# Kernel optimization log

Hardware: AMD Instinct MI355X
Metric: run time of the kernel (lower is better)

## Reference

```python
import jax, jax.numpy as jnp
import numpy as np

WIN = 256  # window_size from init_kwargs


def _stream_attn(q, k, v, win, hollow):
    """Banded sliding-window attention.

    hollow=False (s-stream): key j attended iff 0 <= i - j < win (last `win` tokens incl. self).
    hollow=True  (c-stream): key j attended iff win <= i - j < 2*win (tokens [i-2W+1, i-W]).
    Returns (out [B,S,H,D], lse [B,H,S]) with lse = -inf for fully-masked rows.
    """
    B, S, H, D = q.shape
    nb = S // win
    scale = D ** -0.5
    qb = q.reshape(B, nb, win, H, D)
    kb = k.reshape(B, nb, win, H, D)
    vb = v.reshape(B, nb, win, H, D)
    pad = ((0, 0), (2, 0), (0, 0), (0, 0), (0, 0))
    kp = jnp.pad(kb, pad)
    vp = jnp.pad(vb, pad)
    k_ctx = jnp.concatenate([kp[:, t:t + nb] for t in range(3)], axis=2)  # [B,nb,3W,H,D]
    v_ctx = jnp.concatenate([vp[:, t:t + nb] for t in range(3)], axis=2)
    lq = jnp.arange(win)[:, None]
    kk = jnp.arange(3 * win)[None, :]
    t_blk = kk // win
    lk = kk % win
    rel = (2 - t_blk) * win + lq - lk  # i - j, shape [W, 3W]
    if hollow:
        wmask = (rel >= win) & (rel < 2 * win)
    else:
        wmask = (rel >= 0) & (rel < win)
    blk_ok = (jnp.arange(nb)[:, None] - 2 + (jnp.arange(3 * win) // win)[None, :]) >= 0  # [nb,3W]
    mask = wmask[None] & blk_ok[:, None, :]  # [nb, W, 3W]
    logits = jnp.einsum('bnqhd,bnkhd->bnhqk', qb, k_ctx) * scale  # [B,nb,H,W,3W]
    logits = jnp.where(mask[None, :, None], logits, -jnp.inf)
    m = jnp.max(logits, axis=-1)  # [B,nb,H,W]
    ms = jnp.where(jnp.isneginf(m), 0.0, m)
    p = jnp.exp(logits - ms[..., None])
    denom = jnp.sum(p, axis=-1)  # [B,nb,H,W]
    out = jnp.einsum('bnhqk,bnkhd->bnqhd', p, v_ctx)  # [B,nb,W,H,D]
    safe = jnp.where(denom > 0, denom, 1.0)
    out = out / jnp.moveaxis(safe, 2, 3)[..., None]
    lse = jnp.where(denom > 0, jnp.log(safe) + m, -jnp.inf)  # [B,nb,H,W]
    out = out.reshape(B, S, H, D)
    lse = jnp.moveaxis(lse, 1, 2).reshape(B, H, S)
    return out, lse


def _merge(out_c, lse_c, out_s, lse_s):
    # faithful jax version of merge_attn_states_torch (LSE online-softmax merge)
    m = jnp.maximum(lse_c, lse_s)
    ms = jnp.where(jnp.isneginf(m), 0.0, m)
    ec = jnp.exp(lse_c - ms)
    es = jnp.exp(lse_s - ms)
    se = ec + es  # s-stream always has >=1 key (self), so se > 0
    c_scale = jnp.moveaxis(ec / se, 1, 2)[..., None]  # [B,S,H,1]
    s_scale = jnp.moveaxis(es / se, 1, 2)[..., None]
    return out_c * c_scale + out_s * s_scale


def setup_inputs() -> dict:
    key = jax.random.key(0)
    k1, k2, k3 = jax.random.split(key, 3)
    B, S, H, D = 2, 2048, 16, 128
    return {
        'query': jax.random.normal(k1, (B, S, H, D), dtype=jnp.float32),
        'key': jax.random.normal(k2, (B, S, H, D), dtype=jnp.float32),
        'value': jax.random.normal(k3, (B, S, H, D), dtype=jnp.float32),
    }


def reference(query, key, value):
    out_c, lse_c = _stream_attn(query, key, value, WIN, hollow=True)   # c-stream: [i-2W, i-W]
    out_s, lse_s = _stream_attn(query, key, value, WIN, hollow=False)  # s-stream: last W tokens
    return _merge(out_c, lse_c, out_s, lse_s)
```

## Files before the change

### kernel.cpp

```cpp
#include <hip/hip_runtime.h>
#include <math.h>

#define S_LEN 2048
#define NH    16
#define DD    128
#define SROW  (NH*DD)
#define WIN2  512
#define BQ    128
#define BK    64
#define RSQ   136
#define RS    72

typedef __bf16 bf16x8 __attribute__((ext_vector_type(8)));
typedef __bf16 bf16x4 __attribute__((ext_vector_type(4)));
typedef float  f32x4  __attribute__((ext_vector_type(4)));

__device__ __forceinline__ f32x4 mfma16(bf16x8 a, bf16x8 b, f32x4 c) {
    return __builtin_amdgcn_mfma_f32_16x16x32_bf16(a, b, c, 0, 0, 0);
}

__device__ __forceinline__ unsigned int pack_bf16(float lo, float hi) {
    return (unsigned int)__builtin_bit_cast(unsigned short, (__bf16)lo)
         | ((unsigned int)__builtin_bit_cast(unsigned short, (__bf16)hi) << 16);
}

#define OFF_VT 8704
#define OFF_P  17920
#define SMEM_ELEMS 27136

__global__ __launch_bounds__(256, 2)
void swattn_kernel(const float* __restrict__ Qg, const float* __restrict__ Kg,
                   const float* __restrict__ Vg, float* __restrict__ Og) {
    __shared__ __align__(16) __bf16 smem[SMEM_ELEMS];

    const int t   = threadIdx.x;
    const int w   = t >> 6;
    const int l   = t & 63;
    const int r16 = l & 15;
    const int g4  = l >> 4;
    const int qt  = blockIdx.x;
    const int h   = blockIdx.y;
    const int b   = blockIdx.z;
    const int Qlo = qt * BQ;

    const size_t bh = ((size_t)b * S_LEN) * SROW + (size_t)h * DD;

    for (int it = 0; it < 16; ++it) {
        int f   = it * 256 + t;
        int q_l = f >> 5;
        int dq  = (f & 31) * 4;
        const float4 v = *(const float4*)&Qg[bh + (size_t)(Qlo + q_l) * SROW + dq];
        bf16x4 o4 = { (__bf16)v.x, (__bf16)v.y, (__bf16)v.z, (__bf16)v.w };
        *(bf16x4*)&smem[q_l * RSQ + dq] = o4;
    }
    __syncthreads();

    bf16x8 qf[2][4];
#pragma unroll
    for (int qg = 0; qg < 2; ++qg)
#pragma unroll
        for (int sl = 0; sl < 4; ++sl)
            qf[qg][sl] = *(const bf16x8*)&smem[(w*32 + qg*16 + r16) * RSQ + sl*32 + g4*8];
    __syncthreads();

    const f32x4 zero4 = {0.f, 0.f, 0.f, 0.f};
    f32x4 oacc[8][2];
#pragma unroll
    for (int dg = 0; dg < 8; ++dg) { oacc[dg][0] = zero4; oacc[dg][1] = zero4; }
    float m_run[2] = { -1e30f, -1e30f };
    float l_run[2] = { 0.f, 0.f };

    const int q_lo_w = Qlo + w * 32;
    const int q_hi_w = q_lo_w + 31;
    const float C1 = 0.08838834764831845f * 1.44269504088896340f;

    int cb = Qlo - (WIN2 - 1);
    if (cb < 0) cb = 0;
    cb &= ~(BK - 1);
    const int Qhi = Qlo + BQ - 1;

    for (int c0 = cb; c0 <= Qhi; c0 += BK) {
        for (int it = 0; it < 8; ++it) {
            int f   = it * 256 + t;
            int k_l = f >> 5;
            int dq  = (f & 31) * 4;
            const float4 v = *(const float4*)&Kg[bh + (size_t)(c0 + k_l) * SROW + dq];
            bf16x4 o4 = { (__bf16)v.x, (__bf16)v.y, (__bf16)v.z, (__bf16)v.w };
            *(bf16x4*)&smem[k_l * RSQ + dq] = o4;
        }
        {
            const int gv = l >> 5;
            const int rv = l & 31;
            for (int it = 0; it < 8; ++it) {
                int k0l = w * 16 + it * 2;
                const float4 v4 = *(const float4*)&Vg[bh + (size_t)(c0 + k0l + gv) * SROW + 4*rv];
                float ox = __shfl_xor(v4.x, 32);
                float oy = __shfl_xor(v4.y, 32);
                float oz = __shfl_xor(v4.z, 32);
                float ow = __shfl_xor(v4.w, 32);
                float lo0, hi0, lo1, hi1; int d0;
                if (gv == 0) { lo0 = v4.x; hi0 = ox;   lo1 = v4.y; hi1 = oy;   d0 = 4*rv; }
                else         { lo0 = oz;   hi0 = v4.z; lo1 = ow;   hi1 = v4.w; d0 = 4*rv + 2; }
                *(unsigned int*)&smem[OFF_VT + (d0    ) * RS + k0l] = pack_bf16(lo0, hi0);
                *(unsigned int*)&smem[OFF_VT + (d0 + 1) * RS + k0l] = pack_bf16(lo1, hi1);
            }
        }
        __syncthreads();

        const bool act = (q_hi_w >= c0) && (q_lo_w <= c0 + (BK - 1) + (WIN2 - 1));
        if (act) {
            f32x4 st[4][2];
#pragma unroll
            for (int kg = 0; kg < 4; ++kg) { st[kg][0] = zero4; st[kg][1] = zero4; }
#pragma unroll
            for (int sl = 0; sl < 4; ++sl)
#pragma unroll
                for (int kg = 0; kg < 4; ++kg) {
                    bf16x8 kf = *(const bf16x8*)&smem[(kg*16 + r16) * RSQ + sl*32 + g4*8];
                    st[kg][0] = mfma16(kf, qf[0][sl], st[kg][0]);
                    st[kg][1] = mfma16(kf, qf[1][sl], st[kg][1]);
                }

            const bool fv = (q_lo_w >= c0 + (BK - 1)) && (q_hi_w <= c0 + (WIN2 - 1));
            if (fv) {
#pragma unroll
                for (int kg = 0; kg < 4; ++kg)
#pragma unroll
                    for (int qg = 0; qg < 2; ++qg)
#pragma unroll
                        for (int rg = 0; rg < 4; ++rg) st[kg][qg][rg] *= C1;
            } else {
#pragma unroll
                for (int qg = 0; qg < 2; ++qg) {
                    int iq = q_lo_w + qg*16 + r16;
#pragma unroll
                    for (int kg = 0; kg < 4; ++kg) {
                        int relb = iq - (c0 + kg*16 + 4*g4);
#pragma unroll
                        for (int rg = 0; rg < 4; ++rg) {
                            bool ok = ((unsigned)(relb - rg)) < (unsigned)WIN2;
                            st[kg][qg][rg] = ok ? st[kg][qg][rg] * C1 : -1e30f;
                        }
                    }
                }
            }

            float alpha[2];
#pragma unroll
            for (int qg = 0; qg < 2; ++qg) {
                float mc = -1e30f;
#pragma unroll
                for (int kg = 0; kg < 4; ++kg)
#pragma unroll
                    for (int rg = 0; rg < 4; ++rg) mc = fmaxf(mc, st[kg][qg][rg]);
                mc = fmaxf(mc, __shfl_xor(mc, 16));
                mc = fmaxf(mc, __shfl_xor(mc, 32));
                float mn = fmaxf(m_run[qg], mc);
                alpha[qg] = exp2f(m_run[qg] - mn);
                m_run[qg] = mn;
                float sum = 0.f;
#pragma unroll
                for (int kg = 0; kg < 4; ++kg)
#pragma unroll
                    for (int rg = 0; rg < 4; ++rg) {
                        float tv = st[kg][qg][rg];
                        float p  = exp2f(tv - mn);
                        if (!fv) p = (tv > -1e29f) ? p : 0.f;
                        st[kg][qg][rg] = p;
                        sum += p;
                    }
                sum += __shfl_xor(sum, 16);
                sum += __shfl_xor(sum, 32);
                l_run[qg] = l_run[qg] * alpha[qg] + sum;
            }

#pragma unroll
            for (int qg = 0; qg < 2; ++qg)
#pragma unroll
                for (int kg = 0; kg < 4; ++kg) {
                    f32x4 pv = st[kg][qg];
                    bf16x4 p4 = { (__bf16)pv[0], (__bf16)pv[1], (__bf16)pv[2], (__bf16)pv[3] };
                    *(bf16x4*)&smem[OFF_P + (w*32 + qg*16 + r16) * RS + kg*16 + 4*g4] = p4;
                }

#pragma unroll
            for (int dg = 0; dg < 8; ++dg)
#pragma unroll
                for (int qg = 0; qg < 2; ++qg)
#pragma unroll
                    for (int rg = 0; rg < 4; ++rg) oacc[dg][qg][rg] *= alpha[qg];

#pragma unroll
            for (int ks = 0; ks < 2; ++ks) {
                bf16x8 pf0 = *(const bf16x8*)&smem[OFF_P + (w*32 +  0 + r16) * RS + ks*32 + g4*8];
                bf16x8 pf1 = *(const bf16x8*)&smem[OFF_P + (w*32 + 16 + r16) * RS + ks*32 + g4*8];
#pragma unroll
                for (int dg = 0; dg < 8; ++dg) {
                    bf16x8 vf = *(const bf16x8*)&smem[OFF_VT + (dg*16 + r16) * RS + ks*32 + g4*8];
                    oacc[dg][0] = mfma16(vf, pf0, oacc[dg][0]);
                    oacc[dg][1] = mfma16(vf, pf1, oacc[dg][1]);
                }
            }
        }
        __syncthreads();
    }

    float inv0 = 1.f / l_run[0];
    float inv1 = 1.f / l_run[1];
#pragma unroll
    for (int qg = 0; qg < 2; ++qg) {
        float iv = qg ? inv1 : inv0;
        int q = q_lo_w + qg*16 + r16;
        size_t base = bh + (size_t)q * SROW;
#pragma unroll
        for (int dg = 0; dg < 8; ++dg) {
            f32x4 o = oacc[dg][qg];
            float4 res = { o[0]*iv, o[1]*iv, o[2]*iv, o[3]*iv };
            *(float4*)&Og[base + dg*16 + 4*g4] = res;
        }
    }
}

extern "C" void kernel_launch(void* const* d_in, const int* in_sizes, int n_in,
                              void* d_out, int out_size, void* d_ws, size_t ws_size,
                              hipStream_t stream) {
    const float* q = (const float*)d_in[0];
    const float* k = (const float*)d_in[1];
    const float* v = (const float*)d_in[2];
    float* o = (float*)d_out;
    int B = in_sizes[0] / (S_LEN * NH * DD);
    dim3 grid(S_LEN / BQ, NH, B);
    swattn_kernel<<<grid, 256, 0, stream>>>(q, k, v, o);
}
```

Baseline: 179.4 us.

## Use 8 waves of 16 query rows each, fold scale into Q, swizzle V^T

Doubles the block to 512 threads so each wave owns 16 query rows instead of 32. This halves per-thread accumulators and registers and aims for higher occupancy and better latency hiding. The softmax scale is folded into Q during the bf16 conversion, which removes per-logit multiplies and the masked-probability select; masked entries now rely on exp2 underflow. The V-transpose shared-memory layout gains an XOR swizzle to reduce bank conflicts. The trade-offs are that each K tile is reused by fewer query rows per wave and the launch-bounds target of 4 blocks may not fit the register and shared-memory budget.

```diff
diff --git a/kernel.cpp b/kernel.cpp
--- a/kernel.cpp
+++ b/kernel.cpp
@@ -28,7 +28,7 @@
 #define OFF_P  17920
 #define SMEM_ELEMS 27136
 
-__global__ __launch_bounds__(256, 2)
+__global__ __launch_bounds__(512, 4)
 void swattn_kernel(const float* __restrict__ Qg, const float* __restrict__ Kg,
                    const float* __restrict__ Vg, float* __restrict__ Og) {
     __shared__ __align__(16) __bf16 smem[SMEM_ELEMS];
@@ -38,41 +38,40 @@
     const int l   = t & 63;
     const int r16 = l & 15;
     const int g4  = l >> 4;
-    const int qt  = blockIdx.x;
+    const int Qlo = blockIdx.x * BQ;
     const int h   = blockIdx.y;
     const int b   = blockIdx.z;
-    const int Qlo = qt * BQ;
 
     const size_t bh = ((size_t)b * S_LEN) * SROW + (size_t)h * DD;
-
-    for (int it = 0; it < 16; ++it) {
-        int f   = it * 256 + t;
+    const float C1 = 0.08838834764831845f * 1.44269504088896340f;
+
+    for (int it = 0; it < 8; ++it) {
+        int f   = it * 512 + t;
         int q_l = f >> 5;
         int dq  = (f & 31) * 4;
         const float4 v = *(const float4*)&Qg[bh + (size_t)(Qlo + q_l) * SROW + dq];
-        bf16x4 o4 = { (__bf16)v.x, (__bf16)v.y, (__bf16)v.z, (__bf16)v.w };
+        bf16x4 o4 = { (__bf16)(v.x * C1), (__bf16)(v.y * C1),
+                      (__bf16)(v.z * C1), (__bf16)(v.w * C1) };
         *(bf16x4*)&smem[q_l * RSQ + dq] = o4;
     }
     __syncthreads();
 
-    bf16x8 qf[2][4];
-#pragma unroll
-    for (int qg = 0; qg < 2; ++qg)
-#pragma unroll
-        for (int sl = 0; sl < 4; ++sl)
-            qf[qg][sl] = *(const bf16x8*)&smem[(w*32 + qg*16 + r16) * RSQ + sl*32 + g4*8];
+    bf16x8 qf[4];
+#pragma unroll
+    for (int sl = 0; sl < 4; ++sl)
+        qf[sl] = *(const bf16x8*)&smem[(w*16 + r16) * RSQ + sl*32 + g4*8];
     __syncthreads();
 
     const f32x4 zero4 = {0.f, 0.f, 0.f, 0.f};
-    f32x4 oacc[8][2];
-#pragma unroll
-    for (int dg = 0; dg < 8; ++dg) { oacc[dg][0] = zero4; oacc[dg][1] = zero4; }
-    float m_run[2] = { -1e30f, -1e30f };
-    float l_run[2] = { 0.f, 0.f };
-
-    const int q_lo_w = Qlo + w * 32;
-    const int q_hi_w = q_lo_w + 31;
-    const float C1 = 0.08838834764831845f * 1.44269504088896340f;
+    f32x4 oacc[8];
+#pragma unroll
+    for (int dg = 0; dg < 8; ++dg) oacc[dg] = zero4;
+    float m_run = -1e4f;
+    float l_run = 0.f;
+
+    const int q_w = Qlo + w * 16;
+    const int gv = l >> 5;
+    const int rv = l & 31;
 
     int cb = Qlo - (WIN2 - 1);
     if (cb < 0) cb = 0;
@@ -80,144 +79,112 @@
     const int Qhi = Qlo + BQ - 1;
 
     for (int c0 = cb; c0 <= Qhi; c0 += BK) {
-        for (int it = 0; it < 8; ++it) {
-            int f   = it * 256 + t;
+        for (int it = 0; it < 4; ++it) {
+            int f   = it * 512 + t;
             int k_l = f >> 5;
             int dq  = (f & 31) * 4;
             const float4 v = *(const float4*)&Kg[bh + (size_t)(c0 + k_l) * SROW + dq];
             bf16x4 o4 = { (__bf16)v.x, (__bf16)v.y, (__bf16)v.z, (__bf16)v.w };
             *(bf16x4*)&smem[k_l * RSQ + dq] = o4;
         }
-        {
-            const int gv = l >> 5;
-            const int rv = l & 31;
-            for (int it = 0; it < 8; ++it) {
-                int k0l = w * 16 + it * 2;
-                const float4 v4 = *(const float4*)&Vg[bh + (size_t)(c0 + k0l + gv) * SROW + 4*rv];
-                float ox = __shfl_xor(v4.x, 32);
-                float oy = __shfl_xor(v4.y, 32);
-                float oz = __shfl_xor(v4.z, 32);
-                float ow = __shfl_xor(v4.w, 32);
-                float lo0, hi0, lo1, hi1; int d0;
-                if (gv == 0) { lo0 = v4.x; hi0 = ox;   lo1 = v4.y; hi1 = oy;   d0 = 4*rv; }
-                else         { lo0 = oz;   hi0 = v4.z; lo1 = ow;   hi1 = v4.w; d0 = 4*rv + 2; }
-                *(unsigned int*)&smem[OFF_VT + (d0    ) * RS + k0l] = pack_bf16(lo0, hi0);
-                *(unsigned int*)&smem[OFF_VT + (d0 + 1) * RS + k0l] = pack_bf16(lo1, hi1);
-            }
+        for (int it = 0; it < 4; ++it) {
+            int k0l = w * 8 + it * 2;
+            const float4 v4 = *(const float4*)&Vg[bh + (size_t)(c0 + k0l + gv) * SROW + 4*rv];
+            float ox = __shfl_xor(v4.x, 32);
+            float oy = __shfl_xor(v4.y, 32);
+            float oz = __shfl_xor(v4.z, 32);
+            float ow = __shfl_xor(v4.w, 32);
+            float lo0, hi0, lo1, hi1; int d0;
+            if (gv == 0) { lo0 = v4.x; hi0 = ox;   lo1 = v4.y; hi1 = oy;   d0 = 4*rv; }
+            else         { lo0 = oz;   hi0 = v4.z; lo1 = ow;   hi1 = v4.w; d0 = 4*rv + 2; }
+            int col = k0l ^ ((rv & 7) << 3);
+            *(unsigned int*)&smem[OFF_VT + (d0    ) * RS + col] = pack_bf16(lo0, hi0);
+            *(unsigned int*)&smem[OFF_VT + (d0 + 1) * RS + col] = pack_bf16(lo1, hi1);
         }
         __syncthreads();
 
-        const bool act = (q_hi_w >= c0) && (q_lo_w <= c0 + (BK - 1) + (WIN2 - 1));
+        const bool act = (q_w + 15 >= c0) && (q_w <= c0 + (BK - 1) + (WIN2 - 1));
         if (act) {
-            f32x4 st[4][2];
-#pragma unroll
-            for (int kg = 0; kg < 4; ++kg) { st[kg][0] = zero4; st[kg][1] = zero4; }
+            f32x4 st[4] = { zero4, zero4, zero4, zero4 };
 #pragma unroll
             for (int sl = 0; sl < 4; ++sl)
 #pragma unroll
                 for (int kg = 0; kg < 4; ++kg) {
                     bf16x8 kf = *(const bf16x8*)&smem[(kg*16 + r16) * RSQ + sl*32 + g4*8];
-                    st[kg][0] = mfma16(kf, qf[0][sl], st[kg][0]);
-                    st[kg][1] = mfma16(kf, qf[1][sl], st[kg][1]);
-                }
-
-            const bool fv = (q_lo_w >= c0 + (BK - 1)) && (q_hi_w <= c0 + (WIN2 - 1));
-            if (fv) {
-#pragma unroll
-                for (int kg = 0; kg < 4; ++kg)
-#pragma unroll
-                    for (int qg = 0; qg < 2; ++qg)
-#pragma unroll
-                        for (int rg = 0; rg < 4; ++rg) st[kg][qg][rg] *= C1;
-            } else {
-#pragma unroll
-                for (int qg = 0; qg < 2; ++qg) {
-                    int iq = q_lo_w + qg*16 + r16;
-#pragma unroll
-                    for (int kg = 0; kg < 4; ++kg) {
-                        int relb = iq - (c0 + kg*16 + 4*g4);
-#pragma unroll
-                        for (int rg = 0; rg < 4; ++rg) {
-                            bool ok = ((unsigned)(relb - rg)) < (unsigned)WIN2;
-                            st[kg][qg][rg] = ok ? st[kg][qg][rg] * C1 : -1e30f;
-                        }
+                    st[kg] = mfma16(kf, qf[sl], st[kg]);
+                }
+
+            const bool fv = (q_w >= c0 + (BK - 1)) && (q_w + 15 <= c0 + (WIN2 - 1));
+            if (!fv) {
+                int iq = q_w + r16;
+#pragma unroll
+                for (int kg = 0; kg < 4; ++kg) {
+                    int relb = iq - (c0 + kg*16 + 4*g4);
+#pragma unroll
+                    for (int rg = 0; rg < 4; ++rg) {
+                        bool ok = ((unsigned)(relb - rg)) < (unsigned)WIN2;
+                        st[kg][rg] = ok ? st[kg][rg] : -1e30f;
                     }
                 }
             }
 
-            float alpha[2];
-#pragma unroll
-            for (int qg = 0; qg < 2; ++qg) {
-                float mc = -1e30f;
-#pragma unroll
-                for (int kg = 0; kg < 4; ++kg)
-#pragma unroll
-                    for (int rg = 0; rg < 4; ++rg) mc = fmaxf(mc, st[kg][qg][rg]);
-                mc = fmaxf(mc, __shfl_xor(mc, 16));
-                mc = fmaxf(mc, __shfl_xor(mc, 32));
-                float mn = fmaxf(m_run[qg], mc);
-                alpha[qg] = exp2f(m_run[qg] - mn);
-                m_run[qg] = mn;
-                float sum = 0.f;
-#pragma unroll
-                for (int kg = 0; kg < 4; ++kg)
-#pragma unroll
-                    for (int rg = 0; rg < 4; ++rg) {
-                        float tv = st[kg][qg][rg];
-                        float p  = exp2f(tv - mn);
-                        if (!fv) p = (tv > -1e29f) ? p : 0.f;
-                        st[kg][qg][rg] = p;
-                        sum += p;
-                    }
-                sum += __shfl_xor(sum, 16);
-                sum += __shfl_xor(sum, 32);
-                l_run[qg] = l_run[qg] * alpha[qg] + sum;
+            float mc = -1e30f;
+#pragma unroll
+            for (int kg = 0; kg < 4; ++kg)
+#pragma unroll
+                for (int rg = 0; rg < 4; ++rg) mc = fmaxf(mc, st[kg][rg]);
+            mc = fmaxf(mc, __shfl_xor(mc, 16));
+            mc = fmaxf(mc, __shfl_xor(mc, 32));
+            float mn = fmaxf(m_run, mc);
+            float alpha = exp2f(m_run - mn);
+            m_run = mn;
+            float sum = 0.f;
+#pragma unroll
+            for (int kg = 0; kg < 4; ++kg)
+#pragma unroll
+                for (int rg = 0; rg < 4; ++rg) {
+                    float p = exp2f(st[kg][rg] - mn);
+                    st[kg][rg] = p;
+                    sum += p;
+                }
+            sum += __shfl_xor(sum, 16);
+            sum += __shfl_xor(sum, 32);
+            l_run = l_run * alpha + sum;
+
+#pragma unroll
+            for (int kg = 0; kg < 4; ++kg) {
+                f32x4 pv = st[kg];
+                bf16x4 p4 = { (__bf16)pv[0], (__bf16)pv[1], (__bf16)pv[2], (__bf16)pv[3] };
+                *(bf16x4*)&smem[OFF_P + (w*16 + r16) * RS + kg*16 + 4*g4] = p4;
             }
 
 #pragma unroll
-            for (int qg = 0; qg < 2; ++qg)
-#pragma unroll
-                for (int kg = 0; kg < 4; ++kg) {
-                    f32x4 pv = st[kg][qg];
-                    bf16x4 p4 = { (__bf16)pv[0], (__bf16)pv[1], (__bf16)pv[2], (__bf16)pv[3] };
-                    *(bf16x4*)&smem[OFF_P + (w*32 + qg*16 + r16) * RS + kg*16 + 4*g4] = p4;
-                }
-
-#pragma unroll
             for (int dg = 0; dg < 8; ++dg)
 #pragma unroll
-                for (int qg = 0; qg < 2; ++qg)
-#pragma unroll
-                    for (int rg = 0; rg < 4; ++rg) oacc[dg][qg][rg] *= alpha[qg];
+                for (int rg = 0; rg < 4; ++rg) oacc[dg][rg] *= alpha;
 
 #pragma unroll
             for (int ks = 0; ks < 2; ++ks) {
-                bf16x8 pf0 = *(const bf16x8*)&smem[OFF_P + (w*32 +  0 + r16) * RS + ks*32 + g4*8];
-                bf16x8 pf1 = *(const bf16x8*)&smem[OFF_P + (w*32 + 16 + r16) * RS + ks*32 + g4*8];
+                bf16x8 pf = *(const bf16x8*)&smem[OFF_P + (w*16 + r16) * RS + ks*32 + g4*8];
 #pragma unroll
                 for (int dg = 0; dg < 8; ++dg) {
-                    bf16x8 vf = *(const bf16x8*)&smem[OFF_VT + (dg*16 + r16) * RS + ks*32 + g4*8];
-                    oacc[dg][0] = mfma16(vf, pf0, oacc[dg][0]);
-                    oacc[dg][1] = mfma16(vf, pf1, oacc[dg][1]);
+                    int col = (ks*32 + g4*8) ^ (32*(dg&1) + 8*(r16>>2));
+                    bf16x8 vf = *(const bf16x8*)&smem[OFF_VT + (dg*16 + r16) * RS + col];
+                    oacc[dg] = mfma16(vf, pf, oacc[dg]);
                 }
             }
         }
         __syncthreads();
     }
 
-    float inv0 = 1.f / l_run[0];
-    float inv1 = 1.f / l_run[1];
-#pragma unroll
-    for (int qg = 0; qg < 2; ++qg) {
-        float iv = qg ? inv1 : inv0;
-        int q = q_lo_w + qg*16 + r16;
-        size_t base = bh + (size_t)q * SROW;
-#pragma unroll
-        for (int dg = 0; dg < 8; ++dg) {
-            f32x4 o = oacc[dg][qg];
-            float4 res = { o[0]*iv, o[1]*iv, o[2]*iv, o[3]*iv };
-            *(float4*)&Og[base + dg*16 + 4*g4] = res;
-        }
+    float inv = 1.f / l_run;
+    int q = q_w + r16;
+    size_t base = bh + (size_t)q * SROW;
+#pragma unroll
+    for (int dg = 0; dg < 8; ++dg) {
+        f32x4 o = oacc[dg];
+        float4 res = { o[0]*inv, o[1]*inv, o[2]*inv, o[3]*inv };
+        *(float4*)&Og[base + dg*16 + 4*g4] = res;
     }
 }
 
@@ -230,5 +197,5 @@
     float* o = (float*)d_out;
     int B = in_sizes[0] / (S_LEN * NH * DD);
     dim3 grid(S_LEN / BQ, NH, B);
-    swattn_kernel<<<grid, 256, 0, stream>>>(q, k, v, o);
-}
+    swattn_kernel<<<grid, 512, 0, stream>>>(q, k, v, o);
+}
```

New measurement: 174.8 us. 2.5% less time.
